# Performance work log

Hardware: AMD Instinct MI355X
Metric: run time of the kernel (lower is better)

Reference implementation:

```python
import jax, jax.numpy as jnp
import numpy as np
from jax import lax

A = 20          # alphabet size (input_size)
L = 512         # max_seq_length
CH = 8          # conv channels
N_LAYERS = 9    # log2(512) conv+pool stages


def setup_inputs() -> dict:
    key = jax.random.key(0)
    ks = jax.random.split(key, 6)
    B = 1024
    idx = jax.random.randint(ks[0], (B, L), 0, A)
    lens = jax.random.randint(ks[1], (B,), L // 4, L + 1)
    masks = jnp.arange(L)[None, :] < lens[:, None]            # [B, L] bool
    # one-hot sequences, zeroed at padded positions (so nonzero() skips them)
    x = jax.nn.one_hot(idx, A, dtype=jnp.float32) * masks[..., None].astype(jnp.float32)
    blosum = jax.random.normal(ks[2], (A, A), jnp.float32)
    blosum = (blosum + blosum.T) * 0.5                        # symmetric like BLOSUM
    lpm = blosum                                              # trainable copy
    pm = jnp.clip(blosum, 0.0)                                # clamp(min=0) constant
    std = jnp.ones((1,), jnp.float32)                         # Gaussian std for row decay
    w0 = jax.random.normal(ks[3], (CH, 1, 3), jnp.float32) * 0.3
    ws = jax.random.normal(ks[4], (N_LAYERS - 1, CH, CH, 3), jnp.float32) * 0.2
    return {"x": x, "masks": masks, "lpm": lpm, "pm": pm, "std": std, "w0": w0, "ws": ws}


def _shift_pos(m, k):
    # target index clamp(s + k, max=L-1): shift right by k, boundary index L-1
    # collects any source in the last k+1 positions (set semantics -> OR).
    head = jnp.zeros(m.shape[:-1] + (k,), dtype=bool)
    body = m[..., : L - k - 1]                                # targets k .. L-2
    last = jnp.any(m[..., L - 1 - k:], axis=-1, keepdims=True)
    return jnp.concatenate([head, body, last], axis=-1)


def _shift_neg(m, k):
    # target index clamp(s - k, min=0)
    first = jnp.any(m[..., : k + 1], axis=-1, keepdims=True)
    body = m[..., k + 1:]                                     # targets 1 .. L-1-k
    tail = jnp.zeros(m.shape[:-1] + (k,), dtype=bool)
    return jnp.concatenate([first, body, tail], axis=-1)


def _column(nz, lpm, pm):
    # Banded substitution scatter: each one-hot row i writes V[i, r] into row r
    # at the same (batch, seq) position. Original nested index_put loops collapse
    # to a single 20x20 matrix V applied via einsum (one-hot => no collisions).
    ii = jnp.arange(A)[:, None]
    rr = jnp.arange(A)[None, :]
    M = jnp.clip(lpm, 0.001, 1.0) * pm
    # up-writes: j in 1..18-i => i < r <= 18 ; down-writes: j in 1..i => r < i
    V = jnp.where((rr > ii) & (rr <= A - 2), M, 0.0) + jnp.where(rr < ii, M.T, 0.0)
    return jnp.einsum('bis,ir->brs', nz, V)


def _row(m, std):
    # Gaussian positional decay: writes exp(-k^2/(2 std^2)) at seq offsets +-k,
    # k = 1,2,3 in order (later k overwrites earlier at clamp collisions).
    row = jnp.zeros(m.shape, jnp.float32)
    for k in (1, 2, 3):
        mk = _shift_pos(m, k) | _shift_neg(m, k)
        vk = jnp.exp(-(k * k) / (2.0 * std * std))[0]
        row = jnp.where(mk, vk, row)
    return row


def _conv1d(h, w):
    # Conv1d(kernel=3, stride=1, pad=1, no bias)
    return lax.conv_general_dilated(h, w, (1,), [(1, 1)],
                                    dimension_numbers=('NCH', 'OIH', 'NCH'))


def _avgpool2(h):
    N, C, Lh = h.shape
    return h.reshape(N, C, Lh // 2, 2).mean(-1)


def reference(x, masks, lpm, pm, std, w0, ws):
    B = x.shape[0]
    xp = jnp.transpose(x, (0, 2, 1))          # [B, 20, L]
    m = xp != 0
    nz = m.astype(xp.dtype)
    h = xp + _column(nz, lpm, pm) + _row(m, std)
    h = h.reshape(B * A, 1, L)
    h = _avgpool2(_conv1d(h, w0))
    for i in range(N_LAYERS - 1):
        h = _avgpool2(_conv1d(h, ws[i]))
    return h.squeeze(-1).reshape(B, A, -1)    # [B, 20, 8]
```

## Files before the change

kernel.cpp:

```cpp
#include <hip/hip_runtime.h>
#include <math.h>

#define LSEQ 512
#define NA 20
#define NCH 8
#define NBLK_IMP 129

__global__ __launch_bounds__(256) void wf_vt_kernel(
    const float* __restrict__ w0,
    const float* __restrict__ wsg,
    const float* __restrict__ lpm,
    const float* __restrict__ pm,
    float* __restrict__ wf,
    float* __restrict__ vtn)
{
    if (blockIdx.x == NBLK_IMP) {
        for (int o = threadIdx.x; o < NA * NA; o += 256) {
            int j = o / NA, a = o % NA;
            float v = 0.f;
            if (a > j && a <= NA - 2)
                v += fminf(fmaxf(lpm[j * NA + a], 0.001f), 1.0f) * pm[j * NA + a];
            if (a < j)
                v += fminf(fmaxf(lpm[a * NA + j], 0.001f), 1.0f) * pm[a * NA + j];
            vtn[o] = v;
        }
        return;
    }

    const int w = threadIdx.x >> 6;
    const int t = threadIdx.x & 63;
    const int s = blockIdx.x * 4 + w;

    __shared__ float s_h[4][LSEQ];
    __shared__ float s_a[4][NCH * 256];
    __shared__ float s_b[4][NCH * 128];
    float* hh = s_h[w];
    float* aa = s_a[w];
    float* bb = s_b[w];

    for (int i = t; i < LSEQ; i += 64) hh[i] = (i == s) ? 1.f : 0.f;
    __syncthreads();

    const int c = t >> 3;
    const int pb = t & 7;

    {
        float q0 = w0[c * 3 + 0], q1 = w0[c * 3 + 1], q2 = w0[c * 3 + 2];
        float wa = q0, wb = q0 + q1, wc2 = q1 + q2, wd = q2;
        for (int p = pb; p < 256; p += 8) {
            int xx = 2 * p;
            float x0 = (xx > 0) ? hh[xx - 1] : 0.f;
            float x1 = hh[xx];
            float x2 = hh[xx + 1];
            float x3 = (xx + 2 < LSEQ) ? hh[xx + 2] : 0.f;
            aa[c * 256 + p] = 0.5f * (wa * x0 + wb * x1 + wc2 * x2 + wd * x3);
        }
    }
    __syncthreads();

    int Lin = 256;
    for (int li = 0; li < 8; ++li) {
        const float* fin = (li & 1) ? bb : aa;
        float* fout = (li & 1) ? aa : bb;
        const int Lout = Lin >> 1;

        float wa[8], wb[8], wc2[8], wd[8];
        const float* wl = wsg + li * 192 + c * 24;
#pragma unroll
        for (int ci = 0; ci < 8; ++ci) {
            float q0 = wl[ci * 3 + 0], q1 = wl[ci * 3 + 1], q2 = wl[ci * 3 + 2];
            wa[ci] = q0; wb[ci] = q0 + q1; wc2[ci] = q1 + q2; wd[ci] = q2;
        }

        for (int p = pb; p < Lout; p += 8) {
            int xx = 2 * p;
            float acc = 0.f;
#pragma unroll
            for (int ci = 0; ci < 8; ++ci) {
                const float* ip = fin + ci * Lin + xx;
                float x0 = (xx > 0) ? ip[-1] : 0.f;
                float x1 = ip[0];
                float x2 = ip[1];
                float x3 = (xx + 2 < Lin) ? ip[2] : 0.f;
                acc += wa[ci] * x0 + wb[ci] * x1 + wc2[ci] * x2 + wd[ci] * x3;
            }
            fout[c * Lout + p] = 0.5f * acc;
        }
        __syncthreads();
        Lin = Lout;
    }

    if (t < NCH && s < LSEQ) wf[t * 512 + s] = aa[t];
}

__global__ __launch_bounds__(256) void main_kernel(
    const float* __restrict__ x,
    const float* __restrict__ vtn,
    const float* __restrict__ g_std,
    const float* __restrict__ wf,
    float* __restrict__ out)
{
    const int b = blockIdx.x;
    const int t = threadIdx.x;
    const int c = t & 7;
    const int seg = t >> 3;
    const int w = t >> 6;
    const int lane = t & 63;

    __shared__ __align__(16) float s_h[NA * 512];
    __shared__ __align__(16) float s_vtn[NA * NA];
    __shared__ float s_part[4 * NA * NCH];
    __shared__ unsigned char s_idx[LSEQ];

    float4 wr[4];
#pragma unroll
    for (int k = 0; k < 4; ++k)
        wr[k] = *(const float4*)(wf + c * 512 + seg * 4 + 128 * k);

    if (t < NA * NA / 4) ((float4*)s_vtn)[t] = ((const float4*)vtn)[t];

    const float4* xb = (const float4*)(x + (size_t)b * LSEQ * NA);
#pragma unroll
    for (int rep = 0; rep < 2; ++rep) {
        int s = t + rep * 256;
        int id = 255;
#pragma unroll
        for (int q = 0; q < 5; ++q) {
            float4 v = xb[s * 5 + q];
            if (v.x > .5f) id = 4 * q + 0;
            if (v.y > .5f) id = 4 * q + 1;
            if (v.z > .5f) id = 4 * q + 2;
            if (v.w > .5f) id = 4 * q + 3;
        }
        s_idx[s] = (unsigned char)id;
    }
    __syncthreads();

    const float stdv = g_std[0];
    const float inv2s2 = 1.f / (2.f * stdv * stdv);
    const float vks[3] = {__expf(-1.f * inv2s2), __expf(-4.f * inv2s2), __expf(-9.f * inv2s2)};

    for (int s = t; s < LSEQ; s += 256) {
        const int ai = s_idx[s];
        const bool valid = ai < NA;
#pragma unroll
        for (int a = 0; a < NA; ++a) {
            float v = valid ? (s_vtn[ai * NA + a] + (a == ai ? 1.f : 0.f)) : 0.f;
            s_h[a * 512 + s] = v;
        }
#pragma unroll
        for (int k = 1; k <= 3; ++k) {
            const float add = vks[k - 1];
            if (s == LSEQ - 1) {
                for (int u = LSEQ - 1 - k; u <= LSEQ - 1; ++u) {
                    int tg = s_idx[u];
                    if (tg < NA)
                        s_h[tg * 512 + s] =
                            (valid ? s_vtn[ai * NA + tg] + (tg == ai ? 1.f : 0.f) : 0.f) + add;
                }
            } else if (s >= k) {
                int tg = s_idx[s - k];
                if (tg < NA)
                    s_h[tg * 512 + s] =
                        (valid ? s_vtn[ai * NA + tg] + (tg == ai ? 1.f : 0.f) : 0.f) + add;
            }
            if (s == 0) {
                for (int u = 0; u <= k; ++u) {
                    int tg = s_idx[u];
                    if (tg < NA)
                        s_h[tg * 512 + s] =
                            (valid ? s_vtn[ai * NA + tg] + (tg == ai ? 1.f : 0.f) : 0.f) + add;
                }
            } else if (s + k < LSEQ) {
                int tg = s_idx[s + k];
                if (tg < NA)
                    s_h[tg * 512 + s] =
                        (valid ? s_vtn[ai * NA + tg] + (tg == ai ? 1.f : 0.f) : 0.f) + add;
            }
        }
    }
    __syncthreads();

#pragma unroll 1
    for (int a = 0; a < NA; ++a) {
        const float* hb = s_h + a * 512 + seg * 4;
        float acc = 0.f;
#pragma unroll
        for (int k = 0; k < 4; ++k) {
            float4 hv = *(const float4*)(hb + 128 * k);
            acc += hv.x * wr[k].x + hv.y * wr[k].y + hv.z * wr[k].z + hv.w * wr[k].w;
        }
        acc += __shfl_xor(acc, 8);
        acc += __shfl_xor(acc, 16);
        acc += __shfl_xor(acc, 32);
        if ((lane >> 3) == 0) s_part[w * (NA * NCH) + a * NCH + c] = acc;
    }
    __syncthreads();

    if (t < NA * NCH)
        out[(size_t)b * (NA * NCH) + t] =
            s_part[t] + s_part[160 + t] + s_part[320 + t] + s_part[480 + t];
}

extern "C" void kernel_launch(void* const* d_in, const int* in_sizes, int n_in,
                              void* d_out, int out_size, void* d_ws, size_t ws_size,
                              hipStream_t stream) {
    const float* x    = (const float*)d_in[0];
    const float* lpm  = (const float*)d_in[2];
    const float* pm   = (const float*)d_in[3];
    const float* stdp = (const float*)d_in[4];
    const float* w0   = (const float*)d_in[5];
    const float* wsg  = (const float*)d_in[6];
    float* out = (float*)d_out;

    const int B = in_sizes[0] / (LSEQ * NA);

    float* vtn = (float*)d_ws;
    float* wfb = (float*)d_ws + 1024;

    wf_vt_kernel<<<dim3(NBLK_IMP + 1), dim3(256), 0, stream>>>(w0, wsg, lpm, pm, wfb, vtn);
    main_kernel<<<dim3(B), dim3(256), 0, stream>>>(x, vtn, stdp, wfb, out);
}
```

Before: 124.7 us.

## Move one-hot index decoding into prep kernel and pair channels per thread in dot

Measured after the change: 125.7 us. Within noise of the previous version (+0.8%).

```diff
diff --git a/kernel.cpp b/kernel.cpp
--- a/kernel.cpp
+++ b/kernel.cpp
@@ -5,15 +5,41 @@
 #define NA 20
 #define NCH 8
 #define NBLK_IMP 129
-
-__global__ __launch_bounds__(256) void wf_vt_kernel(
+#define NBLK_PRE (NBLK_IMP + 1)
+
+__global__ __launch_bounds__(256) void prep_kernel(
+    const float* __restrict__ x,
     const float* __restrict__ w0,
     const float* __restrict__ wsg,
     const float* __restrict__ lpm,
     const float* __restrict__ pm,
     float* __restrict__ wf,
-    float* __restrict__ vtn)
+    float* __restrict__ vtn,
+    unsigned char* __restrict__ g_idx)
 {
+    if (blockIdx.x >= NBLK_PRE) {
+        const int b = blockIdx.x - NBLK_PRE;
+        const int t = threadIdx.x;
+        const float4* xb = (const float4*)(x + (size_t)b * LSEQ * NA);
+        unsigned short pack = 0;
+#pragma unroll
+        for (int half = 0; half < 2; ++half) {
+            const int s = 2 * t + half;
+            int id = 255;
+#pragma unroll
+            for (int q = 0; q < 5; ++q) {
+                float4 v = xb[s * 5 + q];
+                if (v.x > .5f) id = 4 * q + 0;
+                if (v.y > .5f) id = 4 * q + 1;
+                if (v.z > .5f) id = 4 * q + 2;
+                if (v.w > .5f) id = 4 * q + 3;
+            }
+            pack |= (unsigned short)(id & 0xFF) << (8 * half);
+        }
+        ((unsigned short*)(g_idx + (size_t)b * LSEQ))[t] = pack;
+        return;
+    }
+
     if (blockIdx.x == NBLK_IMP) {
         for (int o = threadIdx.x; o < NA * NA; o += 256) {
             int j = o / NA, a = o % NA;
@@ -93,8 +119,8 @@
     if (t < NCH && s < LSEQ) wf[t * 512 + s] = aa[t];
 }
 
-__global__ __launch_bounds__(256) void main_kernel(
-    const float* __restrict__ x,
+__global__ __launch_bounds__(256) void dot_kernel(
+    const unsigned char* __restrict__ g_idx,
     const float* __restrict__ vtn,
     const float* __restrict__ g_std,
     const float* __restrict__ wf,
@@ -102,8 +128,8 @@
 {
     const int b = blockIdx.x;
     const int t = threadIdx.x;
-    const int c = t & 7;
-    const int seg = t >> 3;
+    const int cpair = t & 3;
+    const int sge = t >> 2;
     const int w = t >> 6;
     const int lane = t & 63;
 
@@ -112,28 +138,16 @@
     __shared__ float s_part[4 * NA * NCH];
     __shared__ unsigned char s_idx[LSEQ];
 
-    float4 wr[4];
-#pragma unroll
-    for (int k = 0; k < 4; ++k)
-        wr[k] = *(const float4*)(wf + c * 512 + seg * 4 + 128 * k);
-
+    const int c0 = 2 * cpair, c1 = c0 + 1;
+    float4 wr0[2], wr1[2];
+#pragma unroll
+    for (int k = 0; k < 2; ++k) {
+        wr0[k] = *(const float4*)(wf + c0 * 512 + sge * 4 + 256 * k);
+        wr1[k] = *(const float4*)(wf + c1 * 512 + sge * 4 + 256 * k);
+    }
+
+    ((unsigned short*)s_idx)[t] = ((const unsigned short*)(g_idx + (size_t)b * LSEQ))[t];
     if (t < NA * NA / 4) ((float4*)s_vtn)[t] = ((const float4*)vtn)[t];
-
-    const float4* xb = (const float4*)(x + (size_t)b * LSEQ * NA);
-#pragma unroll
-    for (int rep = 0; rep < 2; ++rep) {
-        int s = t + rep * 256;
-        int id = 255;
-#pragma unroll
-        for (int q = 0; q < 5; ++q) {
-            float4 v = xb[s * 5 + q];
-            if (v.x > .5f) id = 4 * q + 0;
-            if (v.y > .5f) id = 4 * q + 1;
-            if (v.z > .5f) id = 4 * q + 2;
-            if (v.w > .5f) id = 4 * q + 3;
-        }
-        s_idx[s] = (unsigned char)id;
-    }
     __syncthreads();
 
     const float stdv = g_std[0];
@@ -183,17 +197,21 @@
 
 #pragma unroll 1
     for (int a = 0; a < NA; ++a) {
-        const float* hb = s_h + a * 512 + seg * 4;
-        float acc = 0.f;
-#pragma unroll
-        for (int k = 0; k < 4; ++k) {
-            float4 hv = *(const float4*)(hb + 128 * k);
-            acc += hv.x * wr[k].x + hv.y * wr[k].y + hv.z * wr[k].z + hv.w * wr[k].w;
-        }
-        acc += __shfl_xor(acc, 8);
-        acc += __shfl_xor(acc, 16);
-        acc += __shfl_xor(acc, 32);
-        if ((lane >> 3) == 0) s_part[w * (NA * NCH) + a * NCH + c] = acc;
+        const float* hb = s_h + a * 512 + sge * 4;
+        float4 h0 = *(const float4*)(hb);
+        float4 h1 = *(const float4*)(hb + 256);
+        float a0 = h0.x * wr0[0].x + h0.y * wr0[0].y + h0.z * wr0[0].z + h0.w * wr0[0].w
+                 + h1.x * wr0[1].x + h1.y * wr0[1].y + h1.z * wr0[1].z + h1.w * wr0[1].w;
+        float a1 = h0.x * wr1[0].x + h0.y * wr1[0].y + h0.z * wr1[0].z + h0.w * wr1[0].w
+                 + h1.x * wr1[1].x + h1.y * wr1[1].y + h1.z * wr1[1].z + h1.w * wr1[1].w;
+        a0 += __shfl_xor(a0, 4);  a1 += __shfl_xor(a1, 4);
+        a0 += __shfl_xor(a0, 8);  a1 += __shfl_xor(a1, 8);
+        a0 += __shfl_xor(a0, 16); a1 += __shfl_xor(a1, 16);
+        a0 += __shfl_xor(a0, 32); a1 += __shfl_xor(a1, 32);
+        if (lane < 4) {
+            s_part[w * (NA * NCH) + a * NCH + c0] = a0;
+            s_part[w * (NA * NCH) + a * NCH + c1] = a1;
+        }
     }
     __syncthreads();
 
@@ -217,7 +235,8 @@
 
     float* vtn = (float*)d_ws;
     float* wfb = (float*)d_ws + 1024;
-
-    wf_vt_kernel<<<dim3(NBLK_IMP + 1), dim3(256), 0, stream>>>(w0, wsg, lpm, pm, wfb, vtn);
-    main_kernel<<<dim3(B), dim3(256), 0, stream>>>(x, vtn, stdp, wfb, out);
+    unsigned char* g_idx = (unsigned char*)d_ws + (1024 + 8 * 512) * 4;
+
+    prep_kernel<<<dim3(NBLK_PRE + B), dim3(256), 0, stream>>>(x, w0, wsg, lpm, pm, wfb, vtn, g_idx);
+    dot_kernel<<<dim3(B), dim3(256), 0, stream>>>(g_idx, vtn, stdp, wfb, out);
 }
```
